# Optimization experiments

Hardware: AMD Instinct MI355X
Metric: run time of the kernel (lower is better)

Reference implementation:

```python
import jax, jax.numpy as jnp
import numpy as np

B, K, C, L = 16, 8, 64, 2048
OFFSET = 2.0  # self.offset in Coupling
EPS = 1e-7    # clamp for logit stability (flows' safe_log analogue)


def setup_inputs() -> dict:
    key = jax.random.key(0)
    ks = jax.random.split(key, 6)
    return {
        "x_change": jax.random.normal(ks[0], (B, C, L), jnp.float32),
        "a": jax.random.normal(ks[1], (B, C, L), jnp.float32),
        "b": jax.random.normal(ks[2], (B, C, L), jnp.float32),
        "pi": jax.random.normal(ks[3], (B, K, C, L), jnp.float32),
        "mu": jax.random.normal(ks[4], (B, K, C, L), jnp.float32),
        "s": jax.random.normal(ks[5], (B, K, C, L), jnp.float32) * 0.1,  # log-scales
        "sldj": jnp.zeros((B,), jnp.float32),
    }


def reference(x_change, a, b, pi, mu, s, sldj):
    # scale = sigmoid(a + offset) + (1 - sigmoid(offset))
    sig_off = 1.0 - jax.nn.sigmoid(jnp.float32(OFFSET))
    scale = jax.nn.sigmoid(a + OFFSET) + sig_off                      # [B,C,L]

    logpi = jax.nn.log_softmax(pi, axis=1)                            # [B,K,C,L]
    z = (x_change[:, None] - mu) * jnp.exp(-s)                        # [B,K,C,L]

    # logistic.mixture_log_cdf: logsumexp_k(log pi_k + log sigmoid(z_k))
    log_cdf = jax.scipy.special.logsumexp(logpi + jax.nn.log_sigmoid(z), axis=1)
    u = jnp.clip(jnp.exp(log_cdf), EPS, 1.0 - EPS)                    # [B,C,L]

    # logistic.inverse (forward): logit, with ldj = -log(u) - log(1-u)
    y = jnp.log(u) - jnp.log1p(-u)
    scale_ldj = -jnp.log(u) - jnp.log1p(-u)

    # logistic.mixture_log_pdf: logsumexp_k(log pi_k + z - s - 2 softplus(z))
    log_pdf = jax.scipy.special.logsumexp(
        logpi + z - s - 2.0 * jax.nn.softplus(z), axis=1)             # [B,C,L]

    sldj_out = sldj + jnp.sum(
        (log_pdf + scale_ldj + jnp.log(scale)).reshape(sldj.shape[0], -1), axis=-1)
    out = (y + b) * scale                                             # [B,C,L]
    return out, sldj_out
```

## Files before the change

### kernel.cpp

```cpp
#include <hip/hip_runtime.h>

#define BB 16
#define KK 8
#define CC 64
#define LL 2048

constexpr int CL = CC * LL;
constexpr int QUADS_PER_BATCH = CL / 4;
constexpr int NBLOCKS = (BB * QUADS_PER_BATCH) / 128;

#define SIG_OFF 0.11920292202211755f
#define LOG_EPS -16.11809565095832f

typedef float f32x4 __attribute__((ext_vector_type(4)));

__device__ __forceinline__ float frcp(float x) { return __builtin_amdgcn_rcpf(x); }

__global__ void init_sldj_kernel(const float* __restrict__ sldj_in,
                                 float* __restrict__ sldj_out) {
    int i = threadIdx.x;
    if (i < BB) sldj_out[i] = sldj_in[i];
}

__global__ __launch_bounds__(256, 4) void coupling_kernel(
    const float* __restrict__ x,
    const float* __restrict__ a,
    const float* __restrict__ bv,
    const float* __restrict__ pi,
    const float* __restrict__ mu,
    const float* __restrict__ s,
    float* __restrict__ out,
    float* __restrict__ sldj_out) {

    const int tid  = threadIdx.x;
    const int lane = tid & 63;
    const int wid  = tid >> 6;
    const int kh   = lane >> 5;
    const int q    = blockIdx.x * 128 + wid * 32 + (lane & 31);
    const int b    = q >> 15;
    const int base = q * 4;
    const int rem4 = base - b * CL;

    const f32x4 x4 = *(const f32x4*)(x + base);

    const int kb0 = (b * KK + kh * 4) * CL + rem4;
    f32x4 pi4[4], mu4[4], s4[4];
#pragma unroll
    for (int j = 0; j < 4; ++j) {
        pi4[j] = *(const f32x4*)(pi + kb0 + j * CL);
        mu4[j] = *(const f32x4*)(mu + kb0 + j * CL);
        s4[j]  = *(const f32x4*)(s  + kb0 + j * CL);
    }
    const f32x4 a4 = *(const f32x4*)(a + base);
    const f32x4 b4 = *(const f32x4*)(bv + base);
    __builtin_amdgcn_sched_barrier(0);

    float Spi[4] = {0.f, 0.f, 0.f, 0.f};
    float Nc[4]  = {0.f, 0.f, 0.f, 0.f};
    float N1[4]  = {0.f, 0.f, 0.f, 0.f};
    float Np[4]  = {0.f, 0.f, 0.f, 0.f};

#pragma unroll
    for (int j = 0; j < 4; ++j) {
#pragma unroll
        for (int e = 0; e < 4; ++e) {
            const float p      = pi4[j][e];
            const float m      = mu4[j][e];
            const float sk     = s4[j][e];
            const float invstd = __expf(-sk);
            const float z      = (x4[e] - m) * invstd;

            const float t  = __expf(-fabsf(z));
            const float r  = frcp(1.f + t);
            const float tr = t * r;
            const float sig  = (z >= 0.f) ? r  : tr;
            const float osig = (z >= 0.f) ? tr : r;

            const float ek = __expf(p);
            Spi[e] += ek;
            Nc[e]  += ek * sig;
            N1[e]  += ek * osig;
            Np[e]  += ek * invstd * sig * osig;
        }
    }

#pragma unroll
    for (int e = 0; e < 4; ++e) {
        Spi[e] += __shfl_xor(Spi[e], 32, 64);
        Nc[e]  += __shfl_xor(Nc[e],  32, 64);
        N1[e]  += __shfl_xor(N1[e],  32, 64);
        Np[e]  += __shfl_xor(Np[e],  32, 64);
    }

    float contrib = 0.f;
    f32x4 out4;

#pragma unroll
    for (int e = 0; e < 4; ++e) {
        const float lSpi = __logf(Spi[e]);
        const float lu   = fmaxf(__logf(Nc[e]) - lSpi, LOG_EPS);
        const float lomu = fmaxf(__logf(N1[e]) - lSpi, LOG_EPS);
        const float y        = lu - lomu;
        const float ldj_term = -lu - lomu;
        const float log_pdf  = __logf(Np[e]) - lSpi;

        const float ae = a4[e] + 2.f;
        const float t2 = __expf(-fabsf(ae));
        const float r2 = frcp(1.f + t2);
        const float sc = ((ae >= 0.f) ? r2 : t2 * r2) + SIG_OFF;

        out4[e] = (y + b4[e]) * sc;
        contrib += log_pdf + ldj_term + __logf(sc);
    }

    if (kh == 0) {
        *(f32x4*)(out + base) = out4;
    } else {
        contrib = 0.f;
    }

#pragma unroll
    for (int off = 32; off > 0; off >>= 1)
        contrib += __shfl_down(contrib, off, 64);

    __shared__ float wsum[4];
    if (lane == 0) wsum[wid] = contrib;
    __syncthreads();
    if (tid == 0) {
        atomicAdd(&sldj_out[b], wsum[0] + wsum[1] + wsum[2] + wsum[3]);
    }
}

extern "C" void kernel_launch(void* const* d_in, const int* in_sizes, int n_in,
                              void* d_out, int out_size, void* d_ws, size_t ws_size,
                              hipStream_t stream) {
    const float* x    = (const float*)d_in[0];
    const float* a    = (const float*)d_in[1];
    const float* bv   = (const float*)d_in[2];
    const float* pi   = (const float*)d_in[3];
    const float* mu   = (const float*)d_in[4];
    const float* s    = (const float*)d_in[5];
    const float* sldj = (const float*)d_in[6];

    float* out      = (float*)d_out;
    float* sldj_out = out + (size_t)BB * CL;

    init_sldj_kernel<<<1, 64, 0, stream>>>(sldj, sldj_out);
    coupling_kernel<<<NBLOCKS, 256, 0, stream>>>(x, a, bv, pi, mu, s, out, sldj_out);
}
```

Before: 224.8 us.

## Issue loads via inline asm with staged vmcnt waits to overlap compute

Replaces the plain vector loads with inline-asm global_load_dwordx4 and inserts explicit s_waitcnt vmcnt waits, so each mixture component group is processed as soon as its own loads land rather than after all 14 loads complete. The a/b loads are waited on only after the mixture reduction. Launch bounds are relaxed from 4 to 2 blocks per SM, giving the compiler more registers. This adds fragile manual wait accounting (the counts must match the load issue order exactly) and may reduce occupancy in a kernel that is memory bound.

Result: no change. 223.0 us (-0.8%).

```diff
diff --git a/kernel.cpp b/kernel.cpp
--- a/kernel.cpp
+++ b/kernel.cpp
@@ -1,4 +1,5 @@
 #include <hip/hip_runtime.h>
+#include <stdint.h>
 
 #define BB 16
 #define KK 8
@@ -16,13 +17,21 @@
 
 __device__ __forceinline__ float frcp(float x) { return __builtin_amdgcn_rcpf(x); }
 
+__device__ __forceinline__ f32x4 gload16(const float* p) {
+    f32x4 r;
+    asm volatile("global_load_dwordx4 %0, %1, off"
+                 : "=v"(r)
+                 : "v"((uint64_t)(uintptr_t)p));
+    return r;
+}
+
 __global__ void init_sldj_kernel(const float* __restrict__ sldj_in,
                                  float* __restrict__ sldj_out) {
     int i = threadIdx.x;
     if (i < BB) sldj_out[i] = sldj_in[i];
 }
 
-__global__ __launch_bounds__(256, 4) void coupling_kernel(
+__global__ __launch_bounds__(256, 2) void coupling_kernel(
     const float* __restrict__ x,
     const float* __restrict__ a,
     const float* __restrict__ bv,
@@ -40,20 +49,18 @@
     const int b    = q >> 15;
     const int base = q * 4;
     const int rem4 = base - b * CL;
+    const int kb0  = (b * KK + kh * 4) * CL + rem4;
 
-    const f32x4 x4 = *(const f32x4*)(x + base);
-
-    const int kb0 = (b * KK + kh * 4) * CL + rem4;
-    f32x4 pi4[4], mu4[4], s4[4];
+    f32x4 x4 = gload16(x + base);
+    f32x4 p4[4], m4[4], s4[4];
 #pragma unroll
     for (int j = 0; j < 4; ++j) {
-        pi4[j] = *(const f32x4*)(pi + kb0 + j * CL);
-        mu4[j] = *(const f32x4*)(mu + kb0 + j * CL);
-        s4[j]  = *(const f32x4*)(s  + kb0 + j * CL);
+        p4[j] = gload16(pi + kb0 + j * CL);
+        m4[j] = gload16(mu + kb0 + j * CL);
+        s4[j] = gload16(s  + kb0 + j * CL);
     }
-    const f32x4 a4 = *(const f32x4*)(a + base);
-    const f32x4 b4 = *(const f32x4*)(bv + base);
-    __builtin_amdgcn_sched_barrier(0);
+    f32x4 a4 = gload16(a + base);
+    f32x4 b4 = gload16(bv + base);
 
     float Spi[4] = {0.f, 0.f, 0.f, 0.f};
     float Nc[4]  = {0.f, 0.f, 0.f, 0.f};
@@ -62,10 +69,23 @@
 
 #pragma unroll
     for (int j = 0; j < 4; ++j) {
+        if (j == 0) {
+            asm volatile("s_waitcnt vmcnt(11)" ::: "memory");
+            asm volatile("" : "+v"(x4));
+        } else if (j == 1) {
+            asm volatile("s_waitcnt vmcnt(8)" ::: "memory");
+        } else if (j == 2) {
+            asm volatile("s_waitcnt vmcnt(5)" ::: "memory");
+        } else {
+            asm volatile("s_waitcnt vmcnt(2)" ::: "memory");
+        }
+        asm volatile("" : "+v"(p4[j]), "+v"(m4[j]), "+v"(s4[j]));
+        __builtin_amdgcn_sched_barrier(0);
+
 #pragma unroll
         for (int e = 0; e < 4; ++e) {
-            const float p      = pi4[j][e];
-            const float m      = mu4[j][e];
+            const float p      = p4[j][e];
+            const float m      = m4[j][e];
             const float sk     = s4[j][e];
             const float invstd = __expf(-sk);
             const float z      = (x4[e] - m) * invstd;
@@ -91,6 +111,10 @@
         N1[e]  += __shfl_xor(N1[e],  32, 64);
         Np[e]  += __shfl_xor(Np[e],  32, 64);
     }
+
+    asm volatile("s_waitcnt vmcnt(0)" ::: "memory");
+    asm volatile("" : "+v"(a4), "+v"(b4));
+    __builtin_amdgcn_sched_barrier(0);
 
     float contrib = 0.f;
     f32x4 out4;
```

## Process 16 elements per thread with full K loop and staggered k order

Applied to the files above, without the earlier changes.

Each thread now handles four quads (16 elements) and loops over all 8 mixture components itself, instead of splitting the components across two half-waves and combining them with shuffles. Blocks start their k loop at a different component based on block index, which spreads concurrent accesses across the pi/mu/s planes. Occupancy hint drops to 2 blocks per CU to allow more registers, and the grid shrinks eightfold. This reduces shuffles, the duplicated x/a/b loads and the number of atomics, at the cost of fewer resident waves to hide memory latency.

Measured after the change: 232.5 us. +3.4%, slower.

```diff
diff --git a/kernel.cpp b/kernel.cpp
--- a/kernel.cpp
+++ b/kernel.cpp
@@ -1,13 +1,15 @@
 #include <hip/hip_runtime.h>
+#include <stdint.h>
 
 #define BB 16
 #define KK 8
 #define CC 64
 #define LL 2048
 
-constexpr int CL = CC * LL;
-constexpr int QUADS_PER_BATCH = CL / 4;
-constexpr int NBLOCKS = (BB * QUADS_PER_BATCH) / 128;
+constexpr int CL  = CC * LL;
+constexpr int QPB = CL / 4;
+constexpr int QBLK = 1024;
+constexpr int NBLOCKS = (BB * QPB) / QBLK;
 
 #define SIG_OFF 0.11920292202211755f
 #define LOG_EPS -16.11809565095832f
@@ -22,7 +24,7 @@
     if (i < BB) sldj_out[i] = sldj_in[i];
 }
 
-__global__ __launch_bounds__(256, 4) void coupling_kernel(
+__global__ __launch_bounds__(256, 2) void coupling_kernel(
     const float* __restrict__ x,
     const float* __restrict__ a,
     const float* __restrict__ bv,
@@ -35,88 +37,87 @@
     const int tid  = threadIdx.x;
     const int lane = tid & 63;
     const int wid  = tid >> 6;
-    const int kh   = lane >> 5;
-    const int q    = blockIdx.x * 128 + wid * 32 + (lane & 31);
-    const int b    = q >> 15;
-    const int base = q * 4;
-    const int rem4 = base - b * CL;
+    const int q0   = blockIdx.x * QBLK + wid * 256 + lane;
+    const int b    = q0 >> 15;
+    const int e0   = q0 * 4;
+    const int rem0 = e0 - b * CL;
 
-    const f32x4 x4 = *(const f32x4*)(x + base);
+    f32x4 x4[4];
+#pragma unroll
+    for (int i = 0; i < 4; ++i) x4[i] = *(const f32x4*)(x + e0 + i * 256);
 
-    const int kb0 = (b * KK + kh * 4) * CL + rem4;
-    f32x4 pi4[4], mu4[4], s4[4];
+    float Spi[4][4], Nc[4][4], N1[4][4], Np[4][4];
 #pragma unroll
-    for (int j = 0; j < 4; ++j) {
-        pi4[j] = *(const f32x4*)(pi + kb0 + j * CL);
-        mu4[j] = *(const f32x4*)(mu + kb0 + j * CL);
-        s4[j]  = *(const f32x4*)(s  + kb0 + j * CL);
-    }
-    const f32x4 a4 = *(const f32x4*)(a + base);
-    const f32x4 b4 = *(const f32x4*)(bv + base);
-    __builtin_amdgcn_sched_barrier(0);
+    for (int i = 0; i < 4; ++i)
+#pragma unroll
+        for (int e = 0; e < 4; ++e) {
+            Spi[i][e] = 0.f; Nc[i][e] = 0.f; N1[i][e] = 0.f; Np[i][e] = 0.f;
+        }
 
-    float Spi[4] = {0.f, 0.f, 0.f, 0.f};
-    float Nc[4]  = {0.f, 0.f, 0.f, 0.f};
-    float N1[4]  = {0.f, 0.f, 0.f, 0.f};
-    float Np[4]  = {0.f, 0.f, 0.f, 0.f};
+    const int kstart = blockIdx.x & 7;
 
 #pragma unroll
-    for (int j = 0; j < 4; ++j) {
+    for (int kk = 0; kk < KK; ++kk) {
+        const int k = (kstart + kk) & (KK - 1);
+        const int kb = (b * KK + k) * CL + rem0;
+
+        f32x4 p4[4], m4[4], s4[4];
 #pragma unroll
-        for (int e = 0; e < 4; ++e) {
-            const float p      = pi4[j][e];
-            const float m      = mu4[j][e];
-            const float sk     = s4[j][e];
-            const float invstd = __expf(-sk);
-            const float z      = (x4[e] - m) * invstd;
+        for (int i = 0; i < 4; ++i) p4[i] = *(const f32x4*)(pi + kb + i * 256);
+#pragma unroll
+        for (int i = 0; i < 4; ++i) m4[i] = *(const f32x4*)(mu + kb + i * 256);
+#pragma unroll
+        for (int i = 0; i < 4; ++i) s4[i] = *(const f32x4*)(s  + kb + i * 256);
 
-            const float t  = __expf(-fabsf(z));
-            const float r  = frcp(1.f + t);
-            const float tr = t * r;
-            const float sig  = (z >= 0.f) ? r  : tr;
-            const float osig = (z >= 0.f) ? tr : r;
+#pragma unroll
+        for (int i = 0; i < 4; ++i) {
+#pragma unroll
+            for (int e = 0; e < 4; ++e) {
+                const float p      = p4[i][e];
+                const float m      = m4[i][e];
+                const float sk     = s4[i][e];
+                const float invstd = __expf(-sk);
+                const float z      = (x4[i][e] - m) * invstd;
 
-            const float ek = __expf(p);
-            Spi[e] += ek;
-            Nc[e]  += ek * sig;
-            N1[e]  += ek * osig;
-            Np[e]  += ek * invstd * sig * osig;
+                const float t  = __expf(-fabsf(z));
+                const float r  = frcp(1.f + t);
+                const float tr = t * r;
+                const float sig  = (z >= 0.f) ? r  : tr;
+                const float osig = (z >= 0.f) ? tr : r;
+
+                const float ek = __expf(p);
+                Spi[i][e] += ek;
+                Nc[i][e]  += ek * sig;
+                N1[i][e]  += ek * osig;
+                Np[i][e]  += ek * invstd * sig * osig;
+            }
         }
     }
 
+    float contrib = 0.f;
 #pragma unroll
-    for (int e = 0; e < 4; ++e) {
-        Spi[e] += __shfl_xor(Spi[e], 32, 64);
-        Nc[e]  += __shfl_xor(Nc[e],  32, 64);
-        N1[e]  += __shfl_xor(N1[e],  32, 64);
-        Np[e]  += __shfl_xor(Np[e],  32, 64);
-    }
+    for (int i = 0; i < 4; ++i) {
+        const f32x4 a4 = *(const f32x4*)(a  + e0 + i * 256);
+        const f32x4 b4 = *(const f32x4*)(bv + e0 + i * 256);
+        f32x4 out4;
+#pragma unroll
+        for (int e = 0; e < 4; ++e) {
+            const float lSpi = __logf(Spi[i][e]);
+            const float lu   = fmaxf(__logf(Nc[i][e]) - lSpi, LOG_EPS);
+            const float lomu = fmaxf(__logf(N1[i][e]) - lSpi, LOG_EPS);
+            const float y        = lu - lomu;
+            const float ldj_term = -lu - lomu;
+            const float log_pdf  = __logf(Np[i][e]) - lSpi;
 
-    float contrib = 0.f;
-    f32x4 out4;
+            const float ae = a4[e] + 2.f;
+            const float t2 = __expf(-fabsf(ae));
+            const float r2 = frcp(1.f + t2);
+            const float sc = ((ae >= 0.f) ? r2 : t2 * r2) + SIG_OFF;
 
-#pragma unroll
-    for (int e = 0; e < 4; ++e) {
-        const float lSpi = __logf(Spi[e]);
-        const float lu   = fmaxf(__logf(Nc[e]) - lSpi, LOG_EPS);
-        const float lomu = fmaxf(__logf(N1[e]) - lSpi, LOG_EPS);
-        const float y        = lu - lomu;
-        const float ldj_term = -lu - lomu;
-        const float log_pdf  = __logf(Np[e]) - lSpi;
-
-        const float ae = a4[e] + 2.f;
-        const float t2 = __expf(-fabsf(ae));
-        const float r2 = frcp(1.f + t2);
-        const float sc = ((ae >= 0.f) ? r2 : t2 * r2) + SIG_OFF;
-
-        out4[e] = (y + b4[e]) * sc;
-        contrib += log_pdf + ldj_term + __logf(sc);
-    }
-
-    if (kh == 0) {
-        *(f32x4*)(out + base) = out4;
-    } else {
-        contrib = 0.f;
+            out4[e] = (y + b4[e]) * sc;
+            contrib += log_pdf + ldj_term + __logf(sc);
+        }
+        *(f32x4*)(out + e0 + i * 256) = out4;
     }
 
 #pragma unroll
```
